# Kernel tuning notes

Hardware: AMD Instinct MI355X
Metric: run time of the kernel (lower is better)

The kernel has to match this reference:

```python
import jax, jax.numpy as jnp
import numpy as np

B = 1024
NQ = 14
NL = 4


def _apply_single(psi_t, gate, q):
    # psi_t: (B, 2, ..., 2) with NQ qubit axes; gate: (2,2) or (B,2,2) complex64
    psi_m = jnp.moveaxis(psi_t, q + 1, -1)
    if gate.ndim == 3:
        new = jnp.einsum('b...i,bji->b...j', psi_m, gate)
    else:
        new = jnp.einsum('b...i,ji->b...j', psi_m, gate)
    return jnp.moveaxis(new, -1, q + 1)


def _apply_cnot(psi_t, c, t):
    # CNOT(control=c, target=t): flip target amplitudes on the control=1 slice
    ca, ta = c + 1, t + 1
    c0 = jax.lax.index_in_dim(psi_t, 0, ca, keepdims=False)
    c1 = jax.lax.index_in_dim(psi_t, 1, ca, keepdims=False)
    ta2 = ta - 1 if ta > ca else ta  # target axis shifts after control axis removal
    c1 = jnp.flip(c1, axis=ta2)  # X on target
    return jnp.stack([c0, c1], axis=ca)


def _forward(inputs, weights):
    Bn, nq = inputs.shape
    nl = weights.shape[0]
    dim = 2 ** nq
    # |0...0> initial state
    psi = jnp.zeros((Bn, dim), dtype=jnp.complex64).at[:, 0].set(1.0)
    psi = psi.reshape((Bn,) + (2,) * nq)
    # RY(theta) per-sample encoding gates: (B, nq, 2, 2)
    c = jnp.cos(inputs / 2).astype(jnp.complex64)
    s = jnp.sin(inputs / 2).astype(jnp.complex64)
    ry = jnp.stack([jnp.stack([c, -s], -1), jnp.stack([s, c], -1)], -2)
    # RX(theta) variational gates: (nl, nq, 2, 2)
    cw = jnp.cos(weights / 2).astype(jnp.complex64)
    sw = jnp.sin(weights / 2).astype(jnp.complex64)
    rx = jnp.stack([jnp.stack([cw, -1j * sw], -1), jnp.stack([-1j * sw, cw], -1)], -2)
    # Encoding layer
    for i in range(nq):
        psi = _apply_single(psi, ry[:, i], i)
    # Variational layers: CNOT chain then RX on every qubit
    for layer in range(nl):
        for i in range(nq - 1):
            psi = _apply_cnot(psi, i, i + 1)
        for i in range(nq):
            psi = _apply_single(psi, rx[layer, i], i)
    # Pauli-Z expectation per qubit
    probs = psi.real ** 2 + psi.imag ** 2  # (B, 2, ..., 2) float32
    exps = []
    for i in range(nq):
        p = jnp.moveaxis(probs, i + 1, 1).reshape(Bn, 2, -1).sum(-1)
        exps.append(p[:, 0] - p[:, 1])
    return jnp.stack(exps, axis=1).astype(jnp.float32)


def setup_inputs() -> dict:
    key = jax.random.key(0)
    k1, k2 = jax.random.split(key)
    inputs = jax.random.normal(k1, (B, NQ), dtype=jnp.float32)
    weights = 0.1 * jax.random.normal(k2, (NL, NQ), dtype=jnp.float32)
    return {"inputs": inputs, "weights": weights}


def reference(inputs, weights):
    return _forward(inputs, weights)
```

## Files before the change

kernel.cpp:

```cpp
#include <hip/hip_runtime.h>
#include <hip/hip_fp16.h>


typedef unsigned int u32;

constexpr int NQ  = 14;
constexpr int DIM = 1 << NQ;
constexpr int NT  = 512;
constexpr int APT = DIM / NT;
constexpr int NL  = 4;

#define H2U(v) __builtin_bit_cast(u32, v)
#define U2H(v) __builtin_bit_cast(__half2, v)
#define DPP1(v) U2H((u32)__builtin_amdgcn_mov_dpp((int)H2U(v), 0xB1, 0xF, 0xF, true))
#define DPP2(v) U2H((u32)__builtin_amdgcn_mov_dpp((int)H2U(v), 0x4E, 0xF, 0xF, true))

#define TB(k) ((t >> (k)) & 1)
#define TM(k) ((Tm >> (k)) & 1)

#define LOADSC(L, Q) { float2 sc_ = wtab[(L) * NQ + (Q)];               \
    sp_ = __floats2half2_rn(sc_.x, -sc_.x);                             \
    cc_ = __float2half2_rn(sc_.y); }

#define RXBIT(ARR, BIT) { _Pragma("unroll")                             \
    for (int o = 0; o < APT; ++o) {                                     \
        if (o & (1 << (BIT))) continue;                                 \
        const int o1_ = o | (1 << (BIT));                               \
        __half2 t0_ = ARR[o], t1_ = ARR[o1_];                           \
        ARR[o]   = __hfma2(sp_, __lowhigh2highlow(t1_), __hmul2(cc_, t0_)); \
        ARR[o1_] = __hfma2(sp_, __lowhigh2highlow(t0_), __hmul2(cc_, t1_)); } }

#define RXD(ARR, DPPM) { _Pragma("unroll")                              \
    for (int o = 0; o < APT; ++o) {                                     \
        __half2 p_ = DPPM(ARR[o]);                                      \
        ARR[o] = __hfma2(sp_, __lowhigh2highlow(p_), __hmul2(cc_, ARR[o])); } }

#define RXLOW(ARR, L)  { __half2 sp_, cc_;                              \
    LOADSC(L,0)  RXBIT(ARR,0) LOADSC(L,1)  RXBIT(ARR,1)                 \
    LOADSC(L,2)  RXBIT(ARR,2) LOADSC(L,3)  RXBIT(ARR,3)                 \
    LOADSC(L,4)  RXBIT(ARR,4) LOADSC(L,5)  RXD(ARR,DPP1)                \
    LOADSC(L,6)  RXD(ARR,DPP2) }
#define RXHIGH(ARR, L) { __half2 sp_, cc_;                              \
    LOADSC(L,7)  RXBIT(ARR,0) LOADSC(L,8)  RXBIT(ARR,1)                 \
    LOADSC(L,9)  RXBIT(ARR,2) LOADSC(L,10) RXBIT(ARR,3)                 \
    LOADSC(L,11) RXBIT(ARR,4) LOADSC(L,12) RXD(ARR,DPP1)                \
    LOADSC(L,13) RXD(ARR,DPP2) }

#define WS1(ARR, BUF) { uint2* b2_ = reinterpret_cast<uint2*>(BUF);     \
    _Pragma("unroll") for (int o = 0; o < APT; o += 2)                  \
        b2_[(CW1 ^ (o | (((o >> 1) & 15) << 10))) >> 1] =               \
            make_uint2(H2U(ARR[o]), H2U(ARR[o + 1])); }
#define RS1(ARR, BUF) { _Pragma("unroll") for (int o = 0; o < APT; ++o) \
        ARR[o] = (BUF)[CR1 ^ (((o & 1) << 3) | (((o >> 1) & 15) << 4))]; }
#define WS2(ARR, BUF) { uint2* b2_ = reinterpret_cast<uint2*>(BUF);     \
    _Pragma("unroll") for (int o = 0; o < APT; o += 2)                  \
        b2_[(CW2 ^ ((o & 15) | (((o >> 4) & 1) << 8) | (((o >> 1) & 7) << 10))) >> 1] = \
            make_uint2(H2U(ARR[o]), H2U(ARR[o + 1])); }
#define RS2(ARR, BUF) { _Pragma("unroll") for (int o = 0; o < APT; ++o) { \
        const int op_ = (o ^ (o << 1)) & 63;                            \
        ARR[o] = (BUF)[CR2 ^ (op_ << 1)]; } }

#define ENCODE(ARR, ROW) {                                              \
    float cs_[NQ], sn_[NQ];                                             \
    _Pragma("unroll") for (int q = 0; q < NQ; ++q)                      \
        __sincosf(0.5f * (ROW)[q], &sn_[q], &cs_[q]);                   \
    float base_ = 1.0f;                                                 \
    _Pragma("unroll") for (int q = 6; q < NQ; ++q)                      \
        base_ *= ((Tm >> (q - 5)) & 1) ? sn_[q] : cs_[q];               \
    _Pragma("unroll") for (int o = 0; o < APT; ++o) {                   \
        const int op_ = o ^ (o << 1);                                   \
        float v_ = base_;                                               \
        _Pragma("unroll") for (int q = 0; q < 5; ++q)                   \
            v_ *= ((op_ >> q) & 1) ? sn_[q] : cs_[q];                   \
        v_ *= (((op_ >> 5) ^ t) & 1) ? sn_[5] : cs_[5];                 \
        ARR[o] = __floats2half2_rn(v_, 0.0f); } }

#define EXPECT(ARR, RED) {                                              \
    float ptot = 0.f, Sq[5] = {0, 0, 0, 0, 0};                          \
    _Pragma("unroll") for (int o = 0; o < APT; ++o) {                   \
        float2 f_ = __half22float2(ARR[o]);                             \
        float p_ = f_.x * f_.x + f_.y * f_.y;                           \
        ptot += p_;                                                     \
        _Pragma("unroll") for (int m = 0; m < 5; ++m)                   \
            Sq[m] += ((o >> m) & 1) ? -p_ : p_; }                       \
    float accL[6];                                                      \
    _Pragma("unroll") for (int k = 0; k < 6; ++k) accL[k] = ptot;       \
    _Pragma("unroll") for (int k = 0; k < 6; ++k) {                     \
        const int m_ = 1 << k;                                          \
        _Pragma("unroll") for (int j = 0; j < 6; ++j) {                 \
            float pr_ = __shfl_xor(accL[j], m_, 64);                    \
            if (j == k) accL[j] = ((lane >> k) & 1) ? (pr_ - accL[j])   \
                                                    : (accL[j] - pr_);  \
            else accL[j] += pr_; }                                      \
        ptot += __shfl_xor(ptot, m_, 64);                               \
        _Pragma("unroll") for (int j2 = 0; j2 < 5; ++j2)                \
            Sq[j2] += __shfl_xor(Sq[j2], m_, 64); }                     \
    if (lane == 0) {                                                    \
        (RED)[wv * 12 + 0] = ptot;                                      \
        _Pragma("unroll") for (int k = 0; k < 6; ++k) (RED)[wv * 12 + 1 + k] = accL[k]; \
        _Pragma("unroll") for (int m2 = 0; m2 < 5; ++m2) (RED)[wv * 12 + 7 + m2] = Sq[m2]; } }

__global__ __launch_bounds__(NT, 2)
void vqc_kernel(const float* __restrict__ inputs,
                const float* __restrict__ weights,
                float* __restrict__ out)
{
    extern __shared__ __half2 lds[];
    const int t    = threadIdx.x;
    const int b    = blockIdx.x;
    const int lane = t & 63;
    const int wv   = t >> 6;
    const int sA   = 2 * b, sB = 2 * b + 1;
    const int Tm   = (t ^ (t << 1)) & 0x3FF;

    __half2* buf0 = lds;
    __half2* buf1 = lds + DIM;
    float2*  wtab = reinterpret_cast<float2*>(lds + 2 * DIM);
    float*   redA = reinterpret_cast<float*>(wtab + 56);
    float*   redB = redA + 96;

    const int CW1 = ((t & 3) << 1) | ((TB(2) ^ TB(8)) << 3) | ((TB(3) ^ TB(7)) << 4)
                  | (((t >> 4) & 7) << 5) | (((t >> 7) & 3) << 8);
    const int CR1 = TB(2) | ((TB(3) ^ TB(7)) << 1) | ((TB(4) ^ TB(8)) << 2)
                  | ((TB(5) ^ TB(1)) << 3) | ((TB(6) ^ TB(0)) << 4)
                  | (TB(0) << 8) | (TB(1) << 9) | (TB(3) << 10) | (TB(4) << 11)
                  | (TB(5) << 12) | (TB(6) << 13);
    const int CW2 = (TB(2) << 1) | (TB(3) << 2) | (TB(4) << 3)
                  | ((TB(5) ^ TB(8) ^ TB(0)) << 4) | (TB(6) << 5) | (TB(7) << 6)
                  | (TB(8) << 7) | (TB(1) << 9) | (TB(0) << 13);
    const int CR2 = TM(2) | (TM(3) << 1) | (TM(4) << 2) | (TM(5) << 3)
                  | ((TM(1) ^ TM(7)) << 4) | (TM(0) << 6) | (TM(1) << 7)
                  | (TM(6) << 8) | (TM(8) << 9) | (TM(3) << 10) | (TM(4) << 11)
                  | (TM(5) << 12) | (TM(7) << 13);

    if (t < NL * NQ) {
        float s_, c_;
        __sincosf(0.5f * weights[t], &s_, &c_);
        wtab[t].x = s_; wtab[t].y = c_;
    }

    __half2 aA[APT], aB[APT];
    ENCODE(aA, inputs + sA * NQ);
    ENCODE(aB, inputs + sB * NQ);
    __syncthreads();

    RXLOW(aA, 0);
    WS1(aA, buf0);                  RXLOW(aB, 0);   __syncthreads();
    RS1(aA, buf0); WS1(aB, buf1);   RXHIGH(aA, 0);  __syncthreads();
    RS1(aB, buf1); WS2(aA, buf0);   RXHIGH(aB, 0);  __syncthreads();

#pragma unroll 1
    for (int l = 1; l < NL; ++l) {
        RS2(aA, buf0); WS2(aB, buf1);  RXLOW(aA, l);   __syncthreads();
        RS2(aB, buf1); WS1(aA, buf0);  RXLOW(aB, l);   __syncthreads();
        RS1(aA, buf0); WS1(aB, buf1);  RXHIGH(aA, l);  __syncthreads();
        RS1(aB, buf1); WS2(aA, buf0);  RXHIGH(aB, l);  __syncthreads();
    }

    EXPECT(aA, redA);
    EXPECT(aB, redB);
    __syncthreads();

    if (t < NQ) {
        float accA = 0.f, accB = 0.f;
#pragma unroll 1
        for (int w = 0; w < 8; ++w) {
            float vA, vB;
            if (t < 4)       { vA = redA[w * 12 + 3 + t];        vB = redB[w * 12 + 3 + t]; }
            else if (t < 7)  { vA = redA[w * 12];                vB = redB[w * 12];
                               if ((w >> (t - 4)) & 1) { vA = -vA; vB = -vB; } }
            else if (t < 12) { vA = redA[w * 12 + 7 + (t - 7)];  vB = redB[w * 12 + 7 + (t - 7)]; }
            else             { vA = redA[w * 12 + 1 + (t - 12)]; vB = redB[w * 12 + 1 + (t - 12)]; }
            accA += vA; accB += vB;
        }
        out[sA * NQ + t] = accA;
        out[sB * NQ + t] = accB;
    }
}

extern "C" void kernel_launch(void* const* d_in, const int* in_sizes, int n_in,
                              void* d_out, int out_size, void* d_ws, size_t ws_size,
                              hipStream_t stream)
{
    const float* inputs  = (const float*)d_in[0];
    const float* weights = (const float*)d_in[1];
    float* out = (float*)d_out;

    const int Bn = in_sizes[0] / NQ;
    const size_t shmem = 2 * DIM * sizeof(__half2) + 56 * sizeof(float2) + 192 * sizeof(float);
    vqc_kernel<<<dim3(Bn / 2), dim3(NT), shmem, stream>>>(inputs, weights, out);
}
```

Baseline: 108.8 us.

## Redesign LDS swizzle layouts, fuse swap into packed FMA, precompute trig tables

```diff
diff --git a/kernel.cpp b/kernel.cpp
--- a/kernel.cpp
+++ b/kernel.cpp
@@ -15,64 +15,81 @@
 #define DPP1(v) U2H((u32)__builtin_amdgcn_mov_dpp((int)H2U(v), 0xB1, 0xF, 0xF, true))
 #define DPP2(v) U2H((u32)__builtin_amdgcn_mov_dpp((int)H2U(v), 0x4E, 0xF, 0xF, true))
 
-#define TB(k) ((t >> (k)) & 1)
-#define TM(k) ((Tm >> (k)) & 1)
-
-#define LOADSC(L, Q) { float2 sc_ = wtab[(L) * NQ + (Q)];               \
-    sp_ = __floats2half2_rn(sc_.x, -sc_.x);                             \
-    cc_ = __float2half2_rn(sc_.y); }
-
-#define RXBIT(ARR, BIT) { _Pragma("unroll")                             \
+static __device__ __forceinline__ __half2 fma_sw(__half2 s, __half2 p, __half2 t) {
+    u32 d, su = H2U(s), pu = H2U(p), tu = H2U(t);
+    asm("v_pk_fma_f16 %0, %1, %2, %3 op_sel:[0,1,0] op_sel_hi:[1,0,1]"
+        : "=v"(d) : "v"(su), "v"(pu), "v"(tu));
+    return U2H(d);
+}
+
+#define LOADSC(L, Q) { uint2 w_ = wtab[(L) * NQ + (Q)];                 \
+    sp_ = U2H(w_.x); cc_ = U2H(w_.y); }
+
+#define RXQ(ARR, QBIT) { _Pragma("unroll")                              \
     for (int o = 0; o < APT; ++o) {                                     \
-        if (o & (1 << (BIT))) continue;                                 \
-        const int o1_ = o | (1 << (BIT));                               \
-        __half2 t0_ = ARR[o], t1_ = ARR[o1_];                           \
-        ARR[o]   = __hfma2(sp_, __lowhigh2highlow(t1_), __hmul2(cc_, t0_)); \
-        ARR[o1_] = __hfma2(sp_, __lowhigh2highlow(t0_), __hmul2(cc_, t1_)); } }
+        if (o & (1 << (QBIT))) continue;                                \
+        const int o1_ = o | (1 << (QBIT));                              \
+        __half2 m0_ = __hmul2(cc_, ARR[o]);                             \
+        __half2 m1_ = __hmul2(cc_, ARR[o1_]);                           \
+        __half2 p0_ = ARR[o1_], p1_ = ARR[o];                           \
+        ARR[o]   = fma_sw(sp_, p0_, m0_);                               \
+        ARR[o1_] = fma_sw(sp_, p1_, m1_); } }
 
 #define RXD(ARR, DPPM) { _Pragma("unroll")                              \
     for (int o = 0; o < APT; ++o) {                                     \
         __half2 p_ = DPPM(ARR[o]);                                      \
-        ARR[o] = __hfma2(sp_, __lowhigh2highlow(p_), __hmul2(cc_, ARR[o])); } }
+        ARR[o] = fma_sw(sp_, p_, __hmul2(cc_, ARR[o])); } }
 
 #define RXLOW(ARR, L)  { __half2 sp_, cc_;                              \
-    LOADSC(L,0)  RXBIT(ARR,0) LOADSC(L,1)  RXBIT(ARR,1)                 \
-    LOADSC(L,2)  RXBIT(ARR,2) LOADSC(L,3)  RXBIT(ARR,3)                 \
-    LOADSC(L,4)  RXBIT(ARR,4) LOADSC(L,5)  RXD(ARR,DPP1)                \
-    LOADSC(L,6)  RXD(ARR,DPP2) }
+    LOADSC(L,0) RXQ(ARR,0) LOADSC(L,1) RXQ(ARR,1) LOADSC(L,2) RXQ(ARR,2)\
+    LOADSC(L,3) RXQ(ARR,3) LOADSC(L,4) RXQ(ARR,4)                       \
+    LOADSC(L,5) RXD(ARR,DPP1) LOADSC(L,6) RXD(ARR,DPP2) }
 #define RXHIGH(ARR, L) { __half2 sp_, cc_;                              \
-    LOADSC(L,7)  RXBIT(ARR,0) LOADSC(L,8)  RXBIT(ARR,1)                 \
-    LOADSC(L,9)  RXBIT(ARR,2) LOADSC(L,10) RXBIT(ARR,3)                 \
-    LOADSC(L,11) RXBIT(ARR,4) LOADSC(L,12) RXD(ARR,DPP1)                \
-    LOADSC(L,13) RXD(ARR,DPP2) }
-
-#define WS1(ARR, BUF) { uint2* b2_ = reinterpret_cast<uint2*>(BUF);     \
-    _Pragma("unroll") for (int o = 0; o < APT; o += 2)                  \
-        b2_[(CW1 ^ (o | (((o >> 1) & 15) << 10))) >> 1] =               \
-            make_uint2(H2U(ARR[o]), H2U(ARR[o + 1])); }
-#define RS1(ARR, BUF) { _Pragma("unroll") for (int o = 0; o < APT; ++o) \
-        ARR[o] = (BUF)[CR1 ^ (((o & 1) << 3) | (((o >> 1) & 15) << 4))]; }
-#define WS2(ARR, BUF) { uint2* b2_ = reinterpret_cast<uint2*>(BUF);     \
-    _Pragma("unroll") for (int o = 0; o < APT; o += 2)                  \
-        b2_[(CW2 ^ ((o & 15) | (((o >> 4) & 1) << 8) | (((o >> 1) & 7) << 10))) >> 1] = \
-            make_uint2(H2U(ARR[o]), H2U(ARR[o + 1])); }
-#define RS2(ARR, BUF) { _Pragma("unroll") for (int o = 0; o < APT; ++o) { \
-        const int op_ = (o ^ (o << 1)) & 63;                            \
-        ARR[o] = (BUF)[CR2 ^ (op_ << 1)]; } }
-
-#define ENCODE(ARR, ROW) {                                              \
-    float cs_[NQ], sn_[NQ];                                             \
-    _Pragma("unroll") for (int q = 0; q < NQ; ++q)                      \
-        __sincosf(0.5f * (ROW)[q], &sn_[q], &cs_[q]);                   \
+    LOADSC(L,7) RXQ(ARR,0) LOADSC(L,8) RXQ(ARR,1) LOADSC(L,9) RXQ(ARR,2)\
+    LOADSC(L,10) RXQ(ARR,3) LOADSC(L,11) RXQ(ARR,4)                     \
+    LOADSC(L,12) RXD(ARR,DPP1) LOADSC(L,13) RXD(ARR,DPP2) }
+
+#define K0(k) ((k)&1)
+#define K1(k) (((k)>>1)&1)
+#define K2(k) (((k)>>2)&1)
+#define K3(k) (((k)>>3)&1)
+#define GW1K(k) ((K0(k)<<3)|(K1(k)<<4)|(K2(k)<<6)|(K3(k)<<7))
+#define GR1K(k) ((K0(k)<<3)|(K1(k)<<4)|(K2(k)<<8)|(K3(k)<<9)|(K0(k)<<12)|(K1(k)<<13))
+#define GW2K(k) ((K0(k)<<1)|(K1(k)<<2)|(K2(k)<<3)|(K3(k)<<4)|(K0(k)<<10)|(K1(k)<<11)|(K2(k)<<12)|(K3(k)<<13))
+#define GR2K(k) (((K0(k)^K1(k))<<3)|((K1(k)^K2(k))<<4)|((K2(k)^K3(k))<<7)|(K3(k)<<8))
+
+#define WS1(ARR, BUF) { _Pragma("unroll") for (int k = 0; k < 16; ++k)  \
+    *reinterpret_cast<uint2*>((BUF) + (CW1x ^ GW1K(k))) =               \
+        make_uint2(H2U(ARR[2*k]), H2U(ARR[2*k+1])); }
+#define RS1(ARR, BUF) { _Pragma("unroll") for (int k = 0; k < 16; ++k) {\
+    const __half2* rp_ = (BUF) + (CR1x ^ GR1K(k));                      \
+    ARR[2*k] = rp_[0]; ARR[2*k+1] = rp_[32]; } }
+#define WS2(ARR, BUF) { _Pragma("unroll") for (int k = 0; k < 16; ++k)  \
+    *reinterpret_cast<uint2*>((BUF) + (CW2x ^ GW2K(k))) =               \
+        make_uint2(H2U(ARR[2*k]), H2U(ARR[2*k+1])); }
+#define RS2(ARR, BUF) { _Pragma("unroll") for (int k = 0; k < 16; ++k) {\
+    const __half2* rp_ = (BUF) + (CR2x ^ GR2K(k));                      \
+    ARR[2*k]   = rp_[(K0(k))<<6];                                       \
+    ARR[2*k+1] = rp_[32 | ((K0(k)^1)<<6)]; } }
+
+#define ENCODE(ARR, TBL) {                                              \
     float base_ = 1.0f;                                                 \
-    _Pragma("unroll") for (int q = 6; q < NQ; ++q)                      \
-        base_ *= ((Tm >> (q - 5)) & 1) ? sn_[q] : cs_[q];               \
+    _Pragma("unroll") for (int q = 6; q < NQ; ++q) {                    \
+        float2 f_ = (TBL)[q];                                           \
+        base_ *= ((Tm >> (q - 5)) & 1) ? f_.x : f_.y; }                 \
+    float2 f5_ = (TBL)[5];                                              \
+    float g5a_ = (t & 1) ? f5_.x : f5_.y;                               \
+    float g5b_ = (t & 1) ? f5_.y : f5_.x;                               \
+    float2 f0_ = (TBL)[0], f1_ = (TBL)[1], f2_ = (TBL)[2],              \
+           f3_ = (TBL)[3], f4_ = (TBL)[4];                              \
     _Pragma("unroll") for (int o = 0; o < APT; ++o) {                   \
         const int op_ = o ^ (o << 1);                                   \
-        float v_ = base_;                                               \
-        _Pragma("unroll") for (int q = 0; q < 5; ++q)                   \
-            v_ *= ((op_ >> q) & 1) ? sn_[q] : cs_[q];                   \
-        v_ *= (((op_ >> 5) ^ t) & 1) ? sn_[5] : cs_[5];                 \
+        float v_ = base_ * ((op_ & 32) ? g5b_ : g5a_);                  \
+        v_ *= (op_ & 1)  ? f0_.x : f0_.y;                               \
+        v_ *= (op_ & 2)  ? f1_.x : f1_.y;                               \
+        v_ *= (op_ & 4)  ? f2_.x : f2_.y;                               \
+        v_ *= (op_ & 8)  ? f3_.x : f3_.y;                               \
+        v_ *= (op_ & 16) ? f4_.x : f4_.y;                               \
         ARR[o] = __floats2half2_rn(v_, 0.0f); } }
 
 #define EXPECT(ARR, RED) {                                              \
@@ -115,47 +132,56 @@
 
     __half2* buf0 = lds;
     __half2* buf1 = lds + DIM;
-    float2*  wtab = reinterpret_cast<float2*>(lds + 2 * DIM);
-    float*   redA = reinterpret_cast<float*>(wtab + 56);
+    uint2*   wtab = reinterpret_cast<uint2*>(lds + 2 * DIM);
+    float2*  itab = reinterpret_cast<float2*>(wtab + 56);
+    float*   redA = reinterpret_cast<float*>(itab + 28);
     float*   redB = redA + 96;
 
-    const int CW1 = ((t & 3) << 1) | ((TB(2) ^ TB(8)) << 3) | ((TB(3) ^ TB(7)) << 4)
-                  | (((t >> 4) & 7) << 5) | (((t >> 7) & 3) << 8);
-    const int CR1 = TB(2) | ((TB(3) ^ TB(7)) << 1) | ((TB(4) ^ TB(8)) << 2)
-                  | ((TB(5) ^ TB(1)) << 3) | ((TB(6) ^ TB(0)) << 4)
-                  | (TB(0) << 8) | (TB(1) << 9) | (TB(3) << 10) | (TB(4) << 11)
-                  | (TB(5) << 12) | (TB(6) << 13);
-    const int CW2 = (TB(2) << 1) | (TB(3) << 2) | (TB(4) << 3)
-                  | ((TB(5) ^ TB(8) ^ TB(0)) << 4) | (TB(6) << 5) | (TB(7) << 6)
-                  | (TB(8) << 7) | (TB(1) << 9) | (TB(0) << 13);
-    const int CR2 = TM(2) | (TM(3) << 1) | (TM(4) << 2) | (TM(5) << 3)
-                  | ((TM(1) ^ TM(7)) << 4) | (TM(0) << 6) | (TM(1) << 7)
-                  | (TM(6) << 8) | (TM(8) << 9) | (TM(3) << 10) | (TM(4) << 11)
-                  | (TM(5) << 12) | (TM(7) << 13);
+    const int t0 = t & 1, t1 = (t >> 1) & 1, t2 = (t >> 2) & 1, t3 = (t >> 3) & 1,
+              t4 = (t >> 4) & 1, t5 = (t >> 5) & 1, t6 = (t >> 6) & 1,
+              t7 = (t >> 7) & 1, t8 = (t >> 8) & 1;
+
+    const int CW1x = ((t0^t7)<<1)|((t1^t8)<<2)|(t3<<3)|(t4<<4)|(t2<<5)
+                   | (t5<<8)|(t6<<9)|(t0<<10)|(t1<<11)|(t3<<12)|(t4<<13);
+    const int CR1x = t2 | ((t7^t0)<<1)|((t8^t1)<<2)|(t3<<3)|(t4<<4)
+                   | (t5<<6)|(t6<<7)|(t7<<10)|(t8<<11);
+    const int CW2x = (t0<<1)|(t1<<2)|(t4<<3)|(t5<<4)|(t2<<5)|(t3<<6)
+                   | (t6<<7)|(t7<<8)|(t8<<9);
+    const int CR2x = (t2^t1) | ((t7^t6^t3^t2)<<1) | ((t8^t7^t4^t3)<<2)
+                   | ((t5^t4)<<3) | ((t6^t5)<<4) | (t0<<8) | ((t1^t0)<<9)
+                   | ((t3^t2)<<10) | ((t4^t3)<<11) | ((t5^t4)<<12) | ((t6^t5)<<13);
 
     if (t < NL * NQ) {
         float s_, c_;
         __sincosf(0.5f * weights[t], &s_, &c_);
-        wtab[t].x = s_; wtab[t].y = c_;
-    }
+        wtab[t] = make_uint2(H2U(__floats2half2_rn(s_, -s_)), H2U(__float2half2_rn(c_)));
+    }
+    if (t >= 64 && t < 64 + 2 * NQ) {
+        int i_ = t - 64;
+        int si_ = (i_ >= NQ) ? 1 : 0;
+        float s_, c_;
+        __sincosf(0.5f * inputs[(sA + si_) * NQ + (i_ - NQ * si_)], &s_, &c_);
+        itab[i_] = make_float2(s_, c_);
+    }
+    __syncthreads();
 
     __half2 aA[APT], aB[APT];
-    ENCODE(aA, inputs + sA * NQ);
-    ENCODE(aB, inputs + sB * NQ);
-    __syncthreads();
-
-    RXLOW(aA, 0);
-    WS1(aA, buf0);                  RXLOW(aB, 0);   __syncthreads();
-    RS1(aA, buf0); WS1(aB, buf1);   RXHIGH(aA, 0);  __syncthreads();
-    RS1(aB, buf1); WS2(aA, buf0);   RXHIGH(aB, 0);  __syncthreads();
+
+    ENCODE(aA, itab);       RXLOW(aA, 0);    WS1(aA, buf0);  __syncthreads();
+    RS1(aA, buf0);  ENCODE(aB, itab + NQ); RXLOW(aB, 0); WS1(aB, buf1); __syncthreads();
+    RS1(aB, buf1);  RXHIGH(aA, 0);  WS2(aA, buf0);  __syncthreads();
+    RS2(aA, buf0);  RXHIGH(aB, 0);  WS2(aB, buf1);  __syncthreads();
 
 #pragma unroll 1
-    for (int l = 1; l < NL; ++l) {
-        RS2(aA, buf0); WS2(aB, buf1);  RXLOW(aA, l);   __syncthreads();
-        RS2(aB, buf1); WS1(aA, buf0);  RXLOW(aB, l);   __syncthreads();
-        RS1(aA, buf0); WS1(aB, buf1);  RXHIGH(aA, l);  __syncthreads();
-        RS1(aB, buf1); WS2(aA, buf0);  RXHIGH(aB, l);  __syncthreads();
-    }
+    for (int l = 1; l < NL - 1; ++l) {
+        RS2(aB, buf1);  RXLOW(aA, l);   WS1(aA, buf0);  __syncthreads();
+        RS1(aA, buf0);  RXLOW(aB, l);   WS1(aB, buf1);  __syncthreads();
+        RS1(aB, buf1);  RXHIGH(aA, l);  WS2(aA, buf0);  __syncthreads();
+        RS2(aA, buf0);  RXHIGH(aB, l);  WS2(aB, buf1);  __syncthreads();
+    }
+    RS2(aB, buf1);  RXLOW(aA, 3);   WS1(aA, buf0);  __syncthreads();
+    RS1(aA, buf0);  RXLOW(aB, 3);   WS1(aB, buf1);  __syncthreads();
+    RS1(aB, buf1);  RXHIGH(aA, 3);  RXHIGH(aB, 3);
 
     EXPECT(aA, redA);
     EXPECT(aB, redB);
@@ -187,6 +213,8 @@
     float* out = (float*)d_out;
 
     const int Bn = in_sizes[0] / NQ;
-    const size_t shmem = 2 * DIM * sizeof(__half2) + 56 * sizeof(float2) + 192 * sizeof(float);
+    const size_t shmem = 2 * DIM * sizeof(__half2)
+                       + 56 * sizeof(uint2) + 28 * sizeof(float2)
+                       + 192 * sizeof(float);
     vqc_kernel<<<dim3(Bn / 2), dim3(NT), shmem, stream>>>(inputs, weights, out);
 }
```

Result: faster. 99.34 us (-8.7%).
